# Kernel optimization log

Measured on AMD Instinct MI355X. Metric: run time of the kernel, lower is better.

The kernel has to match this reference:

```python
import jax, jax.numpy as jnp
import numpy as np
from jax import lax

DIM = 1024
DIM_INNER = 2048  # int(dim * expansion_factor)


def log_g(x):
    # log-space g(x): where(x>=0, log(relu(x)+0.5), -softplus(-x))
    return jnp.where(x >= 0, jnp.log(jax.nn.relu(x) + 0.5), -jax.nn.softplus(-x))


def heinsen_associative_scan_log(log_coeffs, log_values):
    # parallel log-space linear recurrence over the sequence axis (axis=1)
    a_star = jnp.cumsum(log_coeffs, axis=1)
    log_h0_plus_b_star = lax.cumlogsumexp(log_values - a_star, axis=1)
    return a_star + log_h0_plus_b_star


def setup_inputs() -> dict:
    key = jax.random.key(0)
    k_x, k_w1, k_w2 = jax.random.split(key, 3)
    x = jax.random.normal(k_x, (4, 4096, DIM), dtype=jnp.float32)
    # Linear(dim, 2*dim_inner, bias=False): store as [in, out] for x @ W
    W_hg = jax.random.normal(k_w1, (DIM, 2 * DIM_INNER), dtype=jnp.float32) * (1.0 / np.sqrt(DIM))
    W_out = jax.random.normal(k_w2, (DIM_INNER, DIM), dtype=jnp.float32) * (1.0 / np.sqrt(DIM_INNER))
    return {"x": x, "W_hg": W_hg, "W_out": W_out}


def reference(x, W_hg, W_out):
    # x: [b, s, dim]
    hg = jnp.einsum('bsd,de->bse', x, W_hg)  # [b, s, 2*dim_inner]
    hidden, gate = jnp.split(hg, 2, axis=-1)
    log_coeffs = -jax.nn.softplus(gate)        # log(1 - z)
    log_z = -jax.nn.softplus(-gate)            # log z
    log_values = log_z + log_g(hidden)
    log_h = heinsen_associative_scan_log(log_coeffs, log_values)  # [b, s, dim_inner]
    out = jnp.exp(log_h)
    return jnp.einsum('bse,ed->bsd', out, W_out)
```

## Files before the change

kernel.cpp:

```cpp
#include <hip/hip_runtime.h>
#include <cmath>

#define DIM 1024
#define DIM_INNER 2048
#define BATCH 4
#define SEQ 4096
#define MTOT (BATCH * SEQ)
#define CHUNK 32
#define NCHUNK (SEQ / CHUNK)

typedef __bf16 bf16x8 __attribute__((ext_vector_type(8)));
typedef short short8_t __attribute__((ext_vector_type(8)));
typedef float floatx4 __attribute__((ext_vector_type(4)));
typedef unsigned short u16x4 __attribute__((ext_vector_type(4)));
typedef unsigned int uint4_t __attribute__((ext_vector_type(4)));
typedef float float4_t __attribute__((ext_vector_type(4)));
typedef unsigned short ushort_t;

template <int N> struct IC { static constexpr int v = N; };
template <bool B> struct BC { static constexpr bool v = B; };

#define LGKM_SB(n) do { asm volatile("s_waitcnt lgkmcnt(" #n ")" ::: "memory"); \
                        __builtin_amdgcn_sched_barrier(0); } while (0)
#define SCHED0() __builtin_amdgcn_sched_barrier(0)
#define SBAR() __builtin_amdgcn_s_barrier()
#define PRIO1() __builtin_amdgcn_s_setprio(1)
#define PRIO0() __builtin_amdgcn_s_setprio(0)

__device__ __forceinline__ unsigned short f2bf(float f) {
  unsigned int u = __builtin_bit_cast(unsigned int, f);
  u += 0x7fffu + ((u >> 16) & 1u);
  return (unsigned short)(u >> 16);
}
__device__ __forceinline__ float bflo2f(unsigned int u) {
  return __builtin_bit_cast(float, u << 16);
}
__device__ __forceinline__ float bfhi2f(unsigned int u) {
  return __builtin_bit_cast(float, u & 0xffff0000u);
}

__device__ __forceinline__ void lclv_fast(float h, float g, float& lc, float& lv) {
  float eg = __expf(-fabsf(g));
  float sp = fmaxf(g, 0.f) + __logf(1.f + eg);
  lc = -sp;
  float eh = __expf(h);
  float t  = (h >= 0.f) ? (h + 0.5f) : (1.f + eh);
  float lt = __logf(t);
  float lg = (h >= 0.f) ? lt : (h - lt);
  lv = g + lc + lg;
}
__device__ __forceinline__ float logaddexp_f(float a, float b) {
  float m = fmaxf(a, b);
  return m + __logf(1.f + __expf(-fabsf(a - b)));
}

__device__ __forceinline__ void async_copy16(const ushort_t* g, ushort_t* l) {
  __builtin_amdgcn_global_load_lds(
      (const __attribute__((address_space(1))) void*)g,
      (__attribute__((address_space(3))) void*)l, 16, 0, 0);
}

__global__ __launch_bounds__(256) void convert_f32_bf16(
    const float* __restrict__ src, ushort_t* __restrict__ dst) {
  int i = blockIdx.x * 256 + threadIdx.x;
  float4 v = ((const float4*)src)[i];
  u16x4 o = {f2bf(v.x), f2bf(v.y), f2bf(v.z), f2bf(v.w)};
  ((u16x4*)dst)[i] = o;
}

__global__ __launch_bounds__(256) void transpose_f32_bf16(
    const float* __restrict__ src, ushort_t* __restrict__ dst, int K, int N) {
  __shared__ float tile[32][33];
  int tx = threadIdx.x & 31, ty = threadIdx.x >> 5;
  int n0 = blockIdx.x * 32, k0 = blockIdx.y * 32;
#pragma unroll
  for (int i = 0; i < 4; i++) {
    int k = ty + i * 8;
    tile[k][tx] = src[(size_t)(k0 + k) * N + n0 + tx];
  }
  __syncthreads();
#pragma unroll
  for (int i = 0; i < 4; i++) {
    int r = ty + i * 8;
    dst[(size_t)(n0 + r) * K + k0 + tx] = f2bf(tile[tx][r]);
  }
}

#define G1_NT (DIM / 64)
#define G2_NT (DIM_INNER / 64)
#define A0OFF 0
#define A1OFF 16384
#define B0OFF 32768
#define B1OFF 49152

__global__ __launch_bounds__(512, 2) void gemm1_fused(
    const ushort_t* __restrict__ Xbf, const ushort_t* __restrict__ Wt,
    unsigned int* __restrict__ LCLV,
    float* __restrict__ Asum, float* __restrict__ Lend, int nbch) {
  __shared__ __align__(16) ushort_t lds[65536];

  const int tid = threadIdx.x;
  const int lane = tid & 63;
  const int wv = tid >> 6;
  const int wr = wv >> 2;
  const int wc = wv & 3;
  const int l15 = lane & 15;
  const int quad = lane >> 4;
  const int n0 = blockIdx.x * 128;
  const int m0 = blockIdx.y * 256;

  int aSrc[2][2], bSrc[2][2];
  int dstE[2];
#pragma unroll
  for (int L = 0; L < 2; L++) {
    int e = L * 512 + tid;
    int row = e >> 3, slot = e & 7;
    int sw = (slot ^ (row & 7)) << 3;
    dstE[L] = e * 8;
#pragma unroll
    for (int half = 0; half < 2; half++) {
      aSrc[half][L] = (m0 + half * 128 + row) * DIM + sw;
      int br = half * 128 + row;
      int grow = n0 + ((br >> 6) << 5) + (br & 31) + ((br & 32) ? DIM_INNER : 0);
      bSrc[half][L] = grow * DIM + sw;
    }
  }

  auto stA = [&](int kt, int half, auto AO) {
#pragma unroll
    for (int L = 0; L < 2; L++)
      async_copy16(Xbf + aSrc[half][L] + kt * 64,
                   lds + AO.v + half * 8192 + dstE[L]);
  };
  auto stB = [&](int kt, int half, auto BO) {
#pragma unroll
    for (int L = 0; L < 2; L++)
      async_copy16(Wt + bSrc[half][L] + kt * 64,
                   lds + BO.v + half * 8192 + dstE[L]);
  };

  const int swz0 = ((quad ^ (l15 & 7)) << 3);
  const int swz1 = (((4 | quad) ^ (l15 & 7)) << 3);
  const int aB0 = wr * 8192 + l15 * 64 + swz0;
  const int aB1 = wr * 8192 + l15 * 64 + swz1;
  const int bB0 = wc * 4096 + l15 * 64 + swz0;
  const int bB1 = wc * 4096 + l15 * 64 + swz1;

  floatx4 acc[8][4];
#pragma unroll
  for (int i = 0; i < 8; i++)
#pragma unroll
    for (int j = 0; j < 4; j++) acc[i][j] = (floatx4){0.f, 0.f, 0.f, 0.f};

  bf16x8 aF[4][2], b0F[2][2], b1F[2][2];

  auto rdA4 = [&](auto AO, int mb) {
#pragma unroll
    for (int m = 0; m < 4; m++) {
      aF[m][0] = __builtin_bit_cast(bf16x8,
          *(const short8_t*)(lds + AO.v + aB0 + (mb + m) * 1024));
      aF[m][1] = __builtin_bit_cast(bf16x8,
          *(const short8_t*)(lds + AO.v + aB1 + (mb + m) * 1024));
    }
  };
  auto rdB2 = [&](auto BO, int nb, bf16x8 (&bX)[2][2]) {
#pragma unroll
    for (int n = 0; n < 2; n++) {
      bX[n][0] = __builtin_bit_cast(bf16x8,
          *(const short8_t*)(lds + BO.v + bB0 + (nb + n) * 1024));
      bX[n][1] = __builtin_bit_cast(bf16x8,
          *(const short8_t*)(lds + BO.v + bB1 + (nb + n) * 1024));
    }
  };
  auto mmaQ = [&](auto MB, auto JB, bf16x8 (&bX)[2][2]) {
#pragma unroll
    for (int m = 0; m < 4; m++)
#pragma unroll
      for (int jj = 0; jj < 2; jj++)
#pragma unroll
        for (int ks = 0; ks < 2; ks++)
          acc[MB.v + m][JB.v + jj] = __builtin_amdgcn_mfma_f32_16x16x32_bf16(
              aF[m][ks], bX[jj][ks], acc[MB.v + m][JB.v + jj], 0, 0, 0);
  };

  auto pairBody = [&](int k2, auto STG) {
    rdA4(IC<A0OFF>{}, 0); rdB2(IC<B0OFF>{}, 0, b0F);
    SCHED0();
    SBAR(); LGKM_SB(0);
    PRIO1(); mmaQ(IC<0>{}, IC<0>{}, b0F); PRIO0();
    SBAR();
    rdB2(IC<B0OFF>{}, 2, b1F);
    SCHED0();
    SBAR(); LGKM_SB(0);
    PRIO1(); mmaQ(IC<0>{}, IC<2>{}, b1F); PRIO0();
    SBAR();
    rdA4(IC<A0OFF>{}, 4);
    SCHED0();
    if constexpr (STG.v) stB(k2, 0, IC<B0OFF>{});
    SBAR(); LGKM_SB(0);
    PRIO1(); mmaQ(IC<4>{}, IC<2>{}, b1F); PRIO0();
    SBAR();
    if constexpr (STG.v) {
      stB(k2, 1, IC<B0OFF>{});
      asm volatile("s_waitcnt vmcnt(4)" ::: "memory");
    } else {
      asm volatile("s_waitcnt vmcnt(0)" ::: "memory");
    }
    SBAR();
    PRIO1(); mmaQ(IC<4>{}, IC<0>{}, b0F); PRIO0();
    SBAR();
    rdA4(IC<A1OFF>{}, 0); rdB2(IC<B1OFF>{}, 0, b0F);
    SCHED0();
    if constexpr (STG.v) stA(k2, 0, IC<A0OFF>{});
    SBAR(); LGKM_SB(0);
    PRIO1(); mmaQ(IC<0>{}, IC<0>{}, b0F); PRIO0();
    SBAR();
    rdB2(IC<B1OFF>{}, 2, b1F);
    SCHED0();
    if constexpr (STG.v) stA(k2, 1, IC<A0OFF>{});
    SBAR(); LGKM_SB(0);
    PRIO1(); mmaQ(IC<0>{}, IC<2>{}, b1F); PRIO0();
    SBAR();
    rdA4(IC<A1OFF>{}, 4);
    SCHED0();
    if constexpr (STG.v) stB(k2 + 1, 0, IC<B1OFF>{});
    SBAR(); LGKM_SB(0);
    PRIO1(); mmaQ(IC<4>{}, IC<2>{}, b1F); PRIO0();
    SBAR();
    if constexpr (STG.v) {
      stB(k2 + 1, 1, IC<B1OFF>{});
      stA(k2 + 1, 0, IC<A1OFF>{});
      stA(k2 + 1, 1, IC<A1OFF>{});
      asm volatile("s_waitcnt vmcnt(8)" ::: "memory");
    }
    SBAR();
    PRIO1(); mmaQ(IC<4>{}, IC<0>{}, b0F); PRIO0();
    SBAR();
  };

  stA(0, 0, IC<A0OFF>{}); stA(0, 1, IC<A0OFF>{});
  stB(0, 0, IC<B0OFF>{}); stB(0, 1, IC<B0OFF>{});
  stA(1, 0, IC<A1OFF>{}); stA(1, 1, IC<A1OFF>{});
  stB(1, 0, IC<B1OFF>{}); stB(1, 1, IC<B1OFF>{});
  asm volatile("s_waitcnt vmcnt(8)" ::: "memory");
  SBAR();

  for (int it = 0; it < G1_NT / 2 - 1; ++it)
    pairBody(2 * it + 2, BC<true>{});
  pairBody(0, BC<false>{});

#pragma unroll
  for (int c2 = 0; c2 < 4; c2++) {
    float hA[2][2], hL[2][2];
#pragma unroll
    for (int mh = 0; mh < 2; mh++) {
      int mf = c2 * 2 + mh;
#pragma unroll
      for (int j = 0; j < 2; j++) {
        int col = n0 + wc * 32 + j * 16 + l15;
        float sA = 0.f, sL = -INFINITY;
#pragma unroll
        for (int r = 0; r < 4; r++) {
          int row = m0 + wr * 128 + mf * 16 + quad * 4 + r;
          float lc, lv;
          lclv_fast(acc[mf][j][r], acc[mf][j + 2][r], lc, lv);
          unsigned int pk = ((unsigned int)f2bf(lv) << 16) | (unsigned int)f2bf(lc);
          LCLV[(size_t)row * DIM_INNER + col] = pk;
          sL = logaddexp_f(sL + lc, lv);
          sA += lc;
        }
        float A = sA, L = sL;
#pragma unroll
        for (int st = 16; st <= 32; st <<= 1) {
          float Ao = __shfl_xor(A, st, 64);
          float Lo = __shfl_xor(L, st, 64);
          bool upper = (lane & st) != 0;
          L = upper ? logaddexp_f(Lo + A, L) : logaddexp_f(L + Ao, Lo);
          A = A + Ao;
        }
        hA[mh][j] = A;
        hL[mh][j] = L;
      }
    }
#pragma unroll
    for (int j = 0; j < 2; j++) {
      float A = hA[0][j] + hA[1][j];
      float L = logaddexp_f(hL[0][j] + hA[1][j], hL[1][j]);
      if (quad == 0) {
        int cg = (m0 + wr * 128 + c2 * 32) >> 5;
        int bz = cg >> 7;
        int cs = cg & (NCHUNK - 1);
        int col = n0 + wc * 32 + j * 16 + l15;
        size_t sidx = (size_t)cs * nbch + (size_t)bz * DIM_INNER + col;
        Asum[sidx] = A;
        Lend[sidx] = L;
      }
    }
  }
}

__global__ __launch_bounds__(512, 2) void gemm2(
    const ushort_t* __restrict__ Hbf, const ushort_t* __restrict__ Wot,
    float* __restrict__ OUT) {
  __shared__ __align__(16) ushort_t lds[65536];

  const int tid = threadIdx.x;
  const int lane = tid & 63;
  const int wv = tid >> 6;
  const int wr = wv >> 2;
  const int wc = wv & 3;
  const int l15 = lane & 15;
  const int quad = lane >> 4;
  const int n0 = blockIdx.x * 256;
  const int m0 = blockIdx.y * 256;

  int aSrc[2][2], bSrc[2][2];
  int dstE[2];
#pragma unroll
  for (int L = 0; L < 2; L++) {
    int e = L * 512 + tid;
    int row = e >> 3, slot = e & 7;
    int sw = (slot ^ (row & 7)) << 3;
    dstE[L] = e * 8;
#pragma unroll
    for (int half = 0; half < 2; half++) {
      aSrc[half][L] = (m0 + half * 128 + row) * DIM_INNER + sw;
      bSrc[half][L] = (n0 + half * 128 + row) * DIM_INNER + sw;
    }
  }

  auto stA = [&](int kt, int half, auto AO) {
#pragma unroll
    for (int L = 0; L < 2; L++)
      async_copy16(Hbf + aSrc[half][L] + kt * 64,
                   lds + AO.v + half * 8192 + dstE[L]);
  };
  auto stB = [&](int kt, int half, auto BO) {
#pragma unroll
    for (int L = 0; L < 2; L++)
      async_copy16(Wot + bSrc[half][L] + kt * 64,
                   lds + BO.v + half * 8192 + dstE[L]);
  };

  const int swz0 = ((quad ^ (l15 & 7)) << 3);
  const int swz1 = (((4 | quad) ^ (l15 & 7)) << 3);
  const int aB0 = wr * 8192 + l15 * 64 + swz0;
  const int aB1 = wr * 8192 + l15 * 64 + swz1;
  const int bB0 = wc * 4096 + l15 * 64 + swz0;
  const int bB1 = wc * 4096 + l15 * 64 + swz1;

  floatx4 acc[8][4];
#pragma unroll
  for (int i = 0; i < 8; i++)
#pragma unroll
    for (int j = 0; j < 4; j++) acc[i][j] = (floatx4){0.f, 0.f, 0.f, 0.f};

  bf16x8 aF[4][2], b0F[2][2], b1F[2][2];

  auto rdA4 = [&](auto AO, int mb) {
#pragma unroll
    for (int m = 0; m < 4; m++) {
      aF[m][0] = __builtin_bit_cast(bf16x8,
          *(const short8_t*)(lds + AO.v + aB0 + (mb + m) * 1024));
      aF[m][1] = __builtin_bit_cast(bf16x8,
          *(const short8_t*)(lds + AO.v + aB1 + (mb + m) * 1024));
    }
  };
  auto rdB2 = [&](auto BO, int nb, bf16x8 (&bX)[2][2]) {
#pragma unroll
    for (int n = 0; n < 2; n++) {
      bX[n][0] = __builtin_bit_cast(bf16x8,
          *(const short8_t*)(lds + BO.v + bB0 + (nb + n) * 1024));
      bX[n][1] = __builtin_bit_cast(bf16x8,
          *(const short8_t*)(lds + BO.v + bB1 + (nb + n) * 1024));
    }
  };
  auto mmaQ = [&](auto MB, auto JB, bf16x8 (&bX)[2][2]) {
#pragma unroll
    for (int m = 0; m < 4; m++)
#pragma unroll
      for (int jj = 0; jj < 2; jj++)
#pragma unroll
        for (int ks = 0; ks < 2; ks++)
          acc[MB.v + m][JB.v + jj] = __builtin_amdgcn_mfma_f32_16x16x32_bf16(
              aF[m][ks], bX[jj][ks], acc[MB.v + m][JB.v + jj], 0, 0, 0);
  };

  auto pairBody = [&](int k2, auto STG) {
    rdA4(IC<A0OFF>{}, 0); rdB2(IC<B0OFF>{}, 0, b0F);
    SCHED0();
    SBAR(); LGKM_SB(0);
    PRIO1(); mmaQ(IC<0>{}, IC<0>{}, b0F); PRIO0();
    SBAR();
    rdB2(IC<B0OFF>{}, 2, b1F);
    SCHED0();
    SBAR(); LGKM_SB(0);
    PRIO1(); mmaQ(IC<0>{}, IC<2>{}, b1F); PRIO0();
    SBAR();
    rdA4(IC<A0OFF>{}, 4);
    SCHED0();
    if constexpr (STG.v) stB(k2, 0, IC<B0OFF>{});
    SBAR(); LGKM_SB(0);
    PRIO1(); mmaQ(IC<4>{}, IC<2>{}, b1F); PRIO0();
    SBAR();
    if constexpr (STG.v) {
      stB(k2, 1, IC<B0OFF>{});
      asm volatile("s_waitcnt vmcnt(4)" ::: "memory");
    } else {
      asm volatile("s_waitcnt vmcnt(0)" ::: "memory");
    }
    SBAR();
    PRIO1(); mmaQ(IC<4>{}, IC<0>{}, b0F); PRIO0();
    SBAR();
    rdA4(IC<A1OFF>{}, 0); rdB2(IC<B1OFF>{}, 0, b0F);
    SCHED0();
    if constexpr (STG.v) stA(k2, 0, IC<A0OFF>{});
    SBAR(); LGKM_SB(0);
    PRIO1(); mmaQ(IC<0>{}, IC<0>{}, b0F); PRIO0();
    SBAR();
    rdB2(IC<B1OFF>{}, 2, b1F);
    SCHED0();
    if constexpr (STG.v) stA(k2, 1, IC<A0OFF>{});
    SBAR(); LGKM_SB(0);
    PRIO1(); mmaQ(IC<0>{}, IC<2>{}, b1F); PRIO0();
    SBAR();
    rdA4(IC<A1OFF>{}, 4);
    SCHED0();
    if constexpr (STG.v) stB(k2 + 1, 0, IC<B1OFF>{});
    SBAR(); LGKM_SB(0);
    PRIO1(); mmaQ(IC<4>{}, IC<2>{}, b1F); PRIO0();
    SBAR();
    if constexpr (STG.v) {
      stB(k2 + 1, 1, IC<B1OFF>{});
      stA(k2 + 1, 0, IC<A1OFF>{});
      stA(k2 + 1, 1, IC<A1OFF>{});
      asm volatile("s_waitcnt vmcnt(8)" ::: "memory");
    }
    SBAR();
    PRIO1(); mmaQ(IC<4>{}, IC<0>{}, b0F); PRIO0();
    SBAR();
  };

  stA(0, 0, IC<A0OFF>{}); stA(0, 1, IC<A0OFF>{});
  stB(0, 0, IC<B0OFF>{}); stB(0, 1, IC<B0OFF>{});
  stA(1, 0, IC<A1OFF>{}); stA(1, 1, IC<A1OFF>{});
  stB(1, 0, IC<B1OFF>{}); stB(1, 1, IC<B1OFF>{});
  asm volatile("s_waitcnt vmcnt(8)" ::: "memory");
  SBAR();

  for (int it = 0; it < G2_NT / 2 - 1; ++it)
    pairBody(2 * it + 2, BC<true>{});
  pairBody(0, BC<false>{});

#pragma unroll
  for (int mf = 0; mf < 8; mf++)
#pragma unroll
    for (int j = 0; j < 4; j++) {
      int col = n0 + wc * 64 + (j >> 1) * 32 + (j & 1) * 16 + l15;
#pragma unroll
      for (int r = 0; r < 4; r++) {
        int row = m0 + wr * 128 + mf * 16 + quad * 4 + r;
        OUT[(size_t)row * DIM + col] = acc[mf][j][r];
      }
    }
}


__global__ __launch_bounds__(256) void scan_phase2(
    float* Asum, const float* __restrict__ Lend, int nbch) {
  int ch = blockIdx.x * 256 + threadIdx.x;
  float p = -INFINITY;
  for (int c = 0; c < NCHUNK; c++) {
    float a = Asum[(size_t)c * nbch + ch];
    float le = Lend[(size_t)c * nbch + ch];
    Asum[(size_t)c * nbch + ch] = p;
    p = logaddexp_f(a + p, le);
  }
}

__global__ __launch_bounds__(256) void scan_phase3(
    const unsigned int* __restrict__ LCLV, const float* __restrict__ P,
    ushort_t* __restrict__ H, int nbch) {
  const int EQ = DIM_INNER / 4;
  int tid = blockIdx.x * 256 + threadIdx.x;
  int ep = tid % EQ;
  int tmp = tid / EQ;
  int c = tmp % NCHUNK;
  int bz = tmp / NCHUNK;
  size_t base4 = ((size_t)bz * SEQ + (size_t)c * CHUNK) * EQ + ep;
  const uint4_t* L4 = (const uint4_t*)LCLV;
  u16x4* H4 = (u16x4*)H;

  size_t pidx = ((size_t)c * nbch + (size_t)bz * DIM_INNER) / 4 + ep;
  float4_t logh = ((const float4_t*)P)[pidx];
#pragma unroll 4
  for (int t = 0; t < CHUNK; t++) {
    uint4_t u = L4[base4 + (size_t)t * EQ];
    u16x4 hv;
#pragma unroll
    for (int k = 0; k < 4; k++) {
      float lc = bflo2f(u[k]), lv = bfhi2f(u[k]);
      logh[k] = logaddexp_f(lc + logh[k], lv);
      hv[k] = f2bf(__expf(logh[k]));
    }
    H4[base4 + (size_t)t * EQ] = hv;
  }
}

extern "C" void kernel_launch(void* const* d_in, const int* in_sizes, int n_in,
                              void* d_out, int out_size, void* d_ws, size_t ws_size,
                              hipStream_t stream) {
  const float* X = (const float*)d_in[0];
  const float* Whg = (const float*)d_in[1];
  const float* Wout = (const float*)d_in[2];
  float* out = (float*)d_out;

  ushort_t* Xbf = (ushort_t*)d_ws;
  ushort_t* Whg_t = Xbf + (size_t)MTOT * DIM;
  ushort_t* Wout_t = Whg_t + (size_t)(2 * DIM_INNER) * DIM;
  char* pp = (char*)(Wout_t + (size_t)DIM * DIM_INNER);

  const size_t fixed_bytes = (size_t)MTOT * DIM * 2 +
                             (size_t)2 * DIM_INNER * DIM * 2 +
                             (size_t)DIM * DIM_INNER * 2;
  const size_t per_batch = (size_t)SEQ * DIM_INNER * 4 +
                           (size_t)SEQ * DIM_INNER * 2 +
                           2 * (size_t)DIM_INNER * NCHUNK * 4;
  int nb = 4;
  while (nb > 1 && fixed_bytes + (size_t)nb * per_batch > ws_size) nb >>= 1;
  const int npass = BATCH / nb;

  convert_f32_bf16<<<(MTOT * DIM / 4) / 256, 256, 0, stream>>>(X, Xbf);
  transpose_f32_bf16<<<dim3(2 * DIM_INNER / 32, DIM / 32), 256, 0, stream>>>(
      Whg, Whg_t, DIM, 2 * DIM_INNER);
  transpose_f32_bf16<<<dim3(DIM / 32, DIM_INNER / 32), 256, 0, stream>>>(
      Wout, Wout_t, DIM_INNER, DIM);

  for (int pass = 0; pass < npass; pass++) {
    const int b0 = pass * nb;
    const int nrows = nb * SEQ;
    const int nbch = nb * DIM_INNER;

    unsigned int* LCLV = (unsigned int*)pp;
    ushort_t* Hbf = (ushort_t*)(LCLV + (size_t)nb * SEQ * DIM_INNER);
    float* Asum = (float*)(Hbf + (size_t)nb * SEQ * DIM_INNER);
    float* Lend = Asum + (size_t)nb * DIM_INNER * NCHUNK;

    gemm1_fused<<<dim3(DIM_INNER / 128, nrows / 256), 512, 0, stream>>>(
        Xbf + (size_t)b0 * SEQ * DIM, Whg_t, LCLV, Asum, Lend, nbch);
    scan_phase2<<<nbch / 256, 256, 0, stream>>>(Asum, Lend, nbch);
    scan_phase3<<<(nbch / 4 * NCHUNK) / 256, 256, 0, stream>>>(LCLV, Asum, Hbf, nbch);
    gemm2<<<dim3(DIM / 256, nrows / 256), 512, 0, stream>>>(
        Hbf, Wout_t, out + (size_t)b0 * SEQ * DIM);
  }
}
```

Before: 451.5 us.

## Restructure gemm1 main loop with triple-buffered A and finer-grained LDS waits

Rewrites the gemm1_fused K-loop from a double-buffered pair body into a per-tile body that keeps three A buffers and two B buffers in LDS, so A tiles are prefetched two steps ahead. Fragment reads are split per m-row, with staged lgkmcnt waits letting MFMAs start before all LDS reads return. The goal is to hide global-load and LDS latency better. In exchange, LDS use per block grows from 128KB to 160KB, which may limit the two-blocks-per-CU occupancy the launch bounds assume, and it adds runtime buffer-index arithmetic.

New measurement: 447.2 us. About the same (-0.9%).

```diff
diff --git a/kernel.cpp b/kernel.cpp
--- a/kernel.cpp
+++ b/kernel.cpp
@@ -88,20 +88,16 @@
 
 #define G1_NT (DIM / 64)
 #define G2_NT (DIM_INNER / 64)
-#define A0OFF 0
-#define A1OFF 16384
-#define B0OFF 32768
-#define B1OFF 49152
 
 __global__ __launch_bounds__(512, 2) void gemm1_fused(
     const ushort_t* __restrict__ Xbf, const ushort_t* __restrict__ Wt,
     unsigned int* __restrict__ LCLV,
     float* __restrict__ Asum, float* __restrict__ Lend, int nbch) {
-  __shared__ __align__(16) ushort_t lds[65536];
+  __shared__ __align__(16) ushort_t lds[81920];
 
   const int tid = threadIdx.x;
+  const int wv = tid >> 6;
   const int lane = tid & 63;
-  const int wv = tid >> 6;
   const int wr = wv >> 2;
   const int wc = wv & 3;
   const int l15 = lane & 15;
@@ -126,17 +122,17 @@
     }
   }
 
-  auto stA = [&](int kt, int half, auto AO) {
+  auto stageA = [&](int kt, int half, int buf) {
 #pragma unroll
     for (int L = 0; L < 2; L++)
       async_copy16(Xbf + aSrc[half][L] + kt * 64,
-                   lds + AO.v + half * 8192 + dstE[L]);
-  };
-  auto stB = [&](int kt, int half, auto BO) {
+                   lds + buf * 16384 + half * 8192 + dstE[L]);
+  };
+  auto stageB = [&](int kt, int half, int buf) {
 #pragma unroll
     for (int L = 0; L < 2; L++)
       async_copy16(Wt + bSrc[half][L] + kt * 64,
-                   lds + BO.v + half * 8192 + dstE[L]);
+                   lds + 49152 + buf * 16384 + half * 8192 + dstE[L]);
   };
 
   const int swz0 = ((quad ^ (l15 & 7)) << 3);
@@ -146,6 +142,15 @@
   const int bB0 = wc * 4096 + l15 * 64 + swz0;
   const int bB1 = wc * 4096 + l15 * 64 + swz1;
 
+  auto readA = [&](int buf, int mf, int ks) -> bf16x8 {
+    const ushort_t* p = lds + buf * 16384 + (ks ? aB1 : aB0) + mf * 1024;
+    return __builtin_bit_cast(bf16x8, *(const short8_t*)p);
+  };
+  auto readB = [&](int buf, int nf, int ks) -> bf16x8 {
+    const ushort_t* p = lds + 49152 + buf * 16384 + (ks ? bB1 : bB0) + nf * 1024;
+    return __builtin_bit_cast(bf16x8, *(const short8_t*)p);
+  };
+
   floatx4 acc[8][4];
 #pragma unroll
   for (int i = 0; i < 8; i++)
@@ -154,100 +159,109 @@
 
   bf16x8 aF[4][2], b0F[2][2], b1F[2][2];
 
-  auto rdA4 = [&](auto AO, int mb) {
-#pragma unroll
-    for (int m = 0; m < 4; m++) {
-      aF[m][0] = __builtin_bit_cast(bf16x8,
-          *(const short8_t*)(lds + AO.v + aB0 + (mb + m) * 1024));
-      aF[m][1] = __builtin_bit_cast(bf16x8,
-          *(const short8_t*)(lds + AO.v + aB1 + (mb + m) * 1024));
-    }
-  };
-  auto rdB2 = [&](auto BO, int nb, bf16x8 (&bX)[2][2]) {
-#pragma unroll
-    for (int n = 0; n < 2; n++) {
-      bX[n][0] = __builtin_bit_cast(bf16x8,
-          *(const short8_t*)(lds + BO.v + bB0 + (nb + n) * 1024));
-      bX[n][1] = __builtin_bit_cast(bf16x8,
-          *(const short8_t*)(lds + BO.v + bB1 + (nb + n) * 1024));
-    }
-  };
-  auto mmaQ = [&](auto MB, auto JB, bf16x8 (&bX)[2][2]) {
+  auto mma4 = [&](auto MA, auto MC, auto J, bf16x8 (&bX)[2][2]) {
+#pragma unroll
+    for (int jj = 0; jj < 2; jj++)
+#pragma unroll
+      for (int ks = 0; ks < 2; ks++)
+        acc[MC.v][J.v + jj] = __builtin_amdgcn_mfma_f32_16x16x32_bf16(
+            aF[MA.v][ks], bX[jj][ks], acc[MC.v][J.v + jj], 0, 0, 0);
+  };
+  auto mmaRow = [&](auto J, bf16x8 (&bvec)[2]) {
 #pragma unroll
     for (int m = 0; m < 4; m++)
 #pragma unroll
-      for (int jj = 0; jj < 2; jj++)
-#pragma unroll
-        for (int ks = 0; ks < 2; ks++)
-          acc[MB.v + m][JB.v + jj] = __builtin_amdgcn_mfma_f32_16x16x32_bf16(
-              aF[m][ks], bX[jj][ks], acc[MB.v + m][JB.v + jj], 0, 0, 0);
-  };
-
-  auto pairBody = [&](int k2, auto STG) {
-    rdA4(IC<A0OFF>{}, 0); rdB2(IC<B0OFF>{}, 0, b0F);
-    SCHED0();
-    SBAR(); LGKM_SB(0);
-    PRIO1(); mmaQ(IC<0>{}, IC<0>{}, b0F); PRIO0();
-    SBAR();
-    rdB2(IC<B0OFF>{}, 2, b1F);
-    SCHED0();
-    SBAR(); LGKM_SB(0);
-    PRIO1(); mmaQ(IC<0>{}, IC<2>{}, b1F); PRIO0();
-    SBAR();
-    rdA4(IC<A0OFF>{}, 4);
-    SCHED0();
-    if constexpr (STG.v) stB(k2, 0, IC<B0OFF>{});
-    SBAR(); LGKM_SB(0);
-    PRIO1(); mmaQ(IC<4>{}, IC<2>{}, b1F); PRIO0();
-    SBAR();
-    if constexpr (STG.v) {
-      stB(k2, 1, IC<B0OFF>{});
+      for (int ks = 0; ks < 2; ks++)
+        acc[m][J.v] = __builtin_amdgcn_mfma_f32_16x16x32_bf16(
+            aF[m][ks], bvec[ks], acc[m][J.v], 0, 0, 0);
+  };
+
+  int bufA = 0, bufB = 0, bufAn = 2, bufBn = 1;
+
+  auto tileBody = [&](int kb, int ka, auto STB, auto STA, auto VMALL) {
+    aF[0][0] = readA(bufA, 0, 0); aF[0][1] = readA(bufA, 0, 1);
+    b0F[0][0] = readB(bufB, 0, 0); b0F[0][1] = readB(bufB, 0, 1);
+    b0F[1][0] = readB(bufB, 1, 0); b0F[1][1] = readB(bufB, 1, 1);
+    SCHED0();
+    aF[1][0] = readA(bufA, 1, 0); aF[1][1] = readA(bufA, 1, 1);
+    SCHED0();
+    aF[2][0] = readA(bufA, 2, 0); aF[2][1] = readA(bufA, 2, 1);
+    SCHED0();
+    aF[3][0] = readA(bufA, 3, 0); aF[3][1] = readA(bufA, 3, 1);
+    SCHED0();
+    if constexpr (STB.v) stageB(kb, 0, bufBn);
+    SBAR();
+    PRIO1();
+    LGKM_SB(6); mma4(IC<0>{}, IC<0>{}, IC<0>{}, b0F);
+    LGKM_SB(4); mma4(IC<1>{}, IC<1>{}, IC<0>{}, b0F);
+    LGKM_SB(2); mma4(IC<2>{}, IC<2>{}, IC<0>{}, b0F);
+    LGKM_SB(0); mma4(IC<3>{}, IC<3>{}, IC<0>{}, b0F);
+    PRIO0();
+    SBAR();
+
+    b1F[0][0] = readB(bufB, 2, 0); b1F[0][1] = readB(bufB, 2, 1);
+    SCHED0();
+    b1F[1][0] = readB(bufB, 3, 0); b1F[1][1] = readB(bufB, 3, 1);
+    SCHED0();
+    if constexpr (STB.v) stageB(kb, 1, bufBn);
+    SBAR();
+    PRIO1();
+    LGKM_SB(2); mmaRow(IC<2>{}, b1F[0]);
+    LGKM_SB(0); mmaRow(IC<3>{}, b1F[1]);
+    PRIO0();
+    SBAR();
+
+    aF[0][0] = readA(bufA, 4, 0); aF[0][1] = readA(bufA, 4, 1);
+    SCHED0();
+    aF[1][0] = readA(bufA, 5, 0); aF[1][1] = readA(bufA, 5, 1);
+    SCHED0();
+    aF[2][0] = readA(bufA, 6, 0); aF[2][1] = readA(bufA, 6, 1);
+    SCHED0();
+    aF[3][0] = readA(bufA, 7, 0); aF[3][1] = readA(bufA, 7, 1);
+    SCHED0();
+    if constexpr (STA.v) stageA(ka, 0, bufAn);
+    SBAR();
+    PRIO1();
+    LGKM_SB(6); mma4(IC<0>{}, IC<4>{}, IC<2>{}, b1F);
+    LGKM_SB(4); mma4(IC<1>{}, IC<5>{}, IC<2>{}, b1F);
+    LGKM_SB(2); mma4(IC<2>{}, IC<6>{}, IC<2>{}, b1F);
+    LGKM_SB(0); mma4(IC<3>{}, IC<7>{}, IC<2>{}, b1F);
+    PRIO0();
+    SBAR();
+
+    if constexpr (STA.v) stageA(ka, 1, bufAn);
+    SCHED0();
+    if constexpr (STA.v) {
       asm volatile("s_waitcnt vmcnt(4)" ::: "memory");
-    } else {
+    } else if constexpr (VMALL.v) {
       asm volatile("s_waitcnt vmcnt(0)" ::: "memory");
     }
     SBAR();
-    PRIO1(); mmaQ(IC<4>{}, IC<0>{}, b0F); PRIO0();
-    SBAR();
-    rdA4(IC<A1OFF>{}, 0); rdB2(IC<B1OFF>{}, 0, b0F);
-    SCHED0();
-    if constexpr (STG.v) stA(k2, 0, IC<A0OFF>{});
-    SBAR(); LGKM_SB(0);
-    PRIO1(); mmaQ(IC<0>{}, IC<0>{}, b0F); PRIO0();
-    SBAR();
-    rdB2(IC<B1OFF>{}, 2, b1F);
-    SCHED0();
-    if constexpr (STG.v) stA(k2, 1, IC<A0OFF>{});
-    SBAR(); LGKM_SB(0);
-    PRIO1(); mmaQ(IC<0>{}, IC<2>{}, b1F); PRIO0();
-    SBAR();
-    rdA4(IC<A1OFF>{}, 4);
-    SCHED0();
-    if constexpr (STG.v) stB(k2 + 1, 0, IC<B1OFF>{});
-    SBAR(); LGKM_SB(0);
-    PRIO1(); mmaQ(IC<4>{}, IC<2>{}, b1F); PRIO0();
-    SBAR();
-    if constexpr (STG.v) {
-      stB(k2 + 1, 1, IC<B1OFF>{});
-      stA(k2 + 1, 0, IC<A1OFF>{});
-      stA(k2 + 1, 1, IC<A1OFF>{});
-      asm volatile("s_waitcnt vmcnt(8)" ::: "memory");
-    }
-    SBAR();
-    PRIO1(); mmaQ(IC<4>{}, IC<0>{}, b0F); PRIO0();
-    SBAR();
-  };
-
-  stA(0, 0, IC<A0OFF>{}); stA(0, 1, IC<A0OFF>{});
-  stB(0, 0, IC<B0OFF>{}); stB(0, 1, IC<B0OFF>{});
-  stA(1, 0, IC<A1OFF>{}); stA(1, 1, IC<A1OFF>{});
-  stB(1, 0, IC<B1OFF>{}); stB(1, 1, IC<B1OFF>{});
-  asm volatile("s_waitcnt vmcnt(8)" ::: "memory");
+    PRIO1();
+    mma4(IC<0>{}, IC<4>{}, IC<0>{}, b0F);
+    mma4(IC<1>{}, IC<5>{}, IC<0>{}, b0F);
+    mma4(IC<2>{}, IC<6>{}, IC<0>{}, b0F);
+    mma4(IC<3>{}, IC<7>{}, IC<0>{}, b0F);
+    PRIO0();
+    SBAR();
+  };
+
+  stageB(0, 0, 0); stageB(0, 1, 0);
+  stageA(0, 0, 0); stageA(0, 1, 0);
+  stageA(1, 0, 1); stageA(1, 1, 1);
+  asm volatile("s_waitcnt vmcnt(4)" ::: "memory");
   SBAR();
 
-  for (int it = 0; it < G1_NT / 2 - 1; ++it)
-    pairBody(2 * it + 2, BC<true>{});
-  pairBody(0, BC<false>{});
+  for (int u = 0; u < G1_NT - 2; u++) {
+    tileBody(u + 1, u + 2, BC<true>{}, BC<true>{}, BC<false>{});
+    bufA = (bufA == 2) ? 0 : bufA + 1;
+    bufAn = (bufAn == 2) ? 0 : bufAn + 1;
+    bufB ^= 1; bufBn ^= 1;
+  }
+  tileBody(G1_NT - 1, 0, BC<true>{}, BC<false>{}, BC<true>{});
+  bufA = (bufA == 2) ? 0 : bufA + 1;
+  bufB ^= 1;
+  tileBody(0, 0, BC<false>{}, BC<false>{}, BC<false>{});
 
 #pragma unroll
   for (int c2 = 0; c2 < 4; c2++) {
@@ -299,6 +313,11 @@
   }
 }
 
+#define A0OFF 0
+#define A1OFF 16384
+#define B0OFF 32768
+#define B1OFF 49152
+
 __global__ __launch_bounds__(512, 2) void gemm2(
     const ushort_t* __restrict__ Hbf, const ushort_t* __restrict__ Wot,
     float* __restrict__ OUT) {
```
